# Kernel optimization log

Hardware: AMD Instinct MI355X
Metric: run time of the kernel (lower is better)

## Reference

```python
import jax, jax.numpy as jnp
import numpy as np

HIDDEN = 64
IN_SIZE = 2048 + 512  # sum(obs_shape) + sum(action_shape)


def setup_inputs() -> dict:
    key = jax.random.key(0)
    ks = jax.random.split(key, 10)
    B = 32768
    s_in = 1.0 / np.sqrt(IN_SIZE)
    s_h = 1.0 / np.sqrt(HIDDEN)
    return {
        "state": jax.random.normal(ks[0], (B, 2048), dtype=jnp.float32),
        "action": jax.random.normal(ks[1], (B, 512), dtype=jnp.float32),
        "hidden_state": jax.random.normal(ks[2], (B, HIDDEN), dtype=jnp.float32),
        "cell_state": jax.random.normal(ks[3], (B, HIDDEN), dtype=jnp.float32),
        # fused gate weights, gate order: [i, f, g, o]
        "Wi": jax.random.uniform(ks[4], (IN_SIZE, 4 * HIDDEN), jnp.float32, -s_in, s_in),
        "bi": jax.random.uniform(ks[5], (4 * HIDDEN,), jnp.float32, -s_in, s_in),
        "Wh": jax.random.uniform(ks[6], (HIDDEN, 4 * HIDDEN), jnp.float32, -s_h, s_h),
        "bh": jax.random.uniform(ks[7], (4 * HIDDEN,), jnp.float32, -s_h, s_h),
        "Wo": jax.random.uniform(ks[8], (HIDDEN, 1), jnp.float32, -s_h, s_h),
        "bo": jax.random.uniform(ks[9], (1,), jnp.float32, -s_h, s_h),
    }


def reference(state, action, hidden_state, cell_state, Wi, bi, Wh, bh, Wo, bo):
    x = jnp.concatenate([state, action], axis=1)  # [B, IN_SIZE]
    # two fused GEMMs covering all 8 Linear layers (gate order i,f,g,o)
    gates = x @ Wi + bi + hidden_state @ Wh + bh  # [B, 4*HIDDEN]
    i_t, f_t, g_t, o_t = jnp.split(gates, 4, axis=1)
    i_t = jax.nn.sigmoid(i_t)
    f_t = jax.nn.sigmoid(f_t)
    g_t = jnp.tanh(g_t)
    o_t = jax.nn.sigmoid(o_t)
    c_t = f_t * cell_state + i_t * g_t
    h_t = o_t * jnp.tanh(c_t)
    out = jnp.tanh(h_t @ Wo + bo)  # [B, 1]
    return (out, h_t, c_t)
```

## Files before the change

### kernel.cpp

```cpp
#include <hip/hip_runtime.h>
#include <hip/hip_bf16.h>

#define K_IN 2624
#define NSTEP 82
#define NCHUNK 41

typedef __attribute__((ext_vector_type(8))) short short8;
typedef __attribute__((ext_vector_type(4))) float float4_t;

__device__ __forceinline__ short f2bf(float f) {
    union { __hip_bfloat16 b; short s; } u;
    u.b = __float2bfloat16(f);
    return u.s;
}

__device__ __forceinline__ float sigmoid_fast(float x) {
    return 1.f / (1.f + __expf(-x));
}

__device__ __forceinline__ float tanh_fast(float x) {
    float e = __expf(-2.f * fabsf(x));
    float t = (1.f - e) / (1.f + e);
    return copysignf(t, x);
}

__global__ void prep_kernel(const float* __restrict__ Wi, const float* __restrict__ bi,
                            const float* __restrict__ Wh, const float* __restrict__ bh,
                            short* __restrict__ Wt2, float* __restrict__ bsum) {
    __shared__ short tile[32][264];
    const int t = threadIdx.x;
    const int kb = blockIdx.x;
    const int k0 = kb * 32;

#pragma unroll 8
    for (int j = 0; j < 32; ++j) {
        int k = k0 + j;
        float v = (k < 2560) ? Wi[(size_t)k * 256 + t]
                             : Wh[(size_t)(k - 2560) * 256 + t];
        tile[j][t] = f2bf(v);
    }
    if (kb == 0) bsum[t] = bi[t] + bh[t];
    __syncthreads();

#pragma unroll
    for (int c = 0; c < 4; ++c) {
        int idx = c * 256 + t;
        int lane = idx & 63;
        int nb = idx >> 6;
        int n = nb * 16 + (lane & 15);
        int j0 = (lane >> 4) * 8;
        short8 v;
#pragma unroll
        for (int j = 0; j < 8; ++j) v[j] = tile[j0 + j][n];
        *reinterpret_cast<short8*>(Wt2 + (size_t)kb * 8192 + (size_t)idx * 8) = v;
    }
}

__global__ __launch_bounds__(256, 2)
void lstm_kernel(const float* __restrict__ state, const float* __restrict__ action,
                 const float* __restrict__ hidden, const float* __restrict__ cell,
                 const short* __restrict__ Wt2, const float* __restrict__ bsum,
                 const float* __restrict__ Wo, const float* __restrict__ bo,
                 float* __restrict__ out, int Brows) {
    __shared__ __align__(16) short sB[2 * 16384];

    const int t = threadIdx.x;
    const int w = t >> 6;
    const int l = t & 63;
    const int lr = l & 15;
    const int q = l >> 4;
    const int bm = blockIdx.x;

    const size_t mrow = (size_t)bm * 64 + w * 16 + lr;
    const float* aS = state  + mrow * 2048;
    const float* aA = action + mrow * 512;
    const float* aH = hidden + mrow * 64;

    const short* bg = Wt2 + t * 8;

    float4_t acc[16];
#pragma unroll
    for (int nb = 0; nb < 16; ++nb) acc[nb] = (float4_t)(0.f);

    float4_t aCur[4], aNxt[4], bReg[8];

    auto loadA = [&](int c, float4_t* dst) {
        const float* p; int col;
        if (c < 32)      { p = aS; col = c * 64; }
        else if (c < 40) { p = aA; col = (c - 32) * 64; }
        else             { p = aH; col = 0; }
        dst[0] = *reinterpret_cast<const float4_t*>(p + col + q * 8);
        dst[1] = *reinterpret_cast<const float4_t*>(p + col + q * 8 + 4);
        dst[2] = *reinterpret_cast<const float4_t*>(p + col + 32 + q * 8);
        dst[3] = *reinterpret_cast<const float4_t*>(p + col + 32 + q * 8 + 4);
    };
    auto loadB = [&](int c) {
#pragma unroll
        for (int i = 0; i < 8; ++i)
            bReg[i] = *reinterpret_cast<const float4_t*>(bg + (size_t)c * 16384 + i * 2048);
    };
    auto storeB = [&](int c) {
        short* d = sB + (c & 1) * 16384 + t * 8;
#pragma unroll
        for (int i = 0; i < 8; ++i)
            *reinterpret_cast<float4_t*>(d + i * 2048) = bReg[i];
    };

    loadB(0);
    loadA(0, aCur);
    loadA(1, aNxt);
    storeB(0);
    __syncthreads();

    for (int k = 0; k < NCHUNK; ++k) {
        if (k + 1 < NCHUNK) loadB(k + 1);

        const short* bufr = sB + (k & 1) * 16384;
#pragma unroll
        for (int s = 0; s < 2; ++s) {
            short8 a;
            a[0] = f2bf(aCur[2*s][0]); a[1] = f2bf(aCur[2*s][1]);
            a[2] = f2bf(aCur[2*s][2]); a[3] = f2bf(aCur[2*s][3]);
            a[4] = f2bf(aCur[2*s+1][0]); a[5] = f2bf(aCur[2*s+1][1]);
            a[6] = f2bf(aCur[2*s+1][2]); a[7] = f2bf(aCur[2*s+1][3]);
#pragma unroll
            for (int nb = 0; nb < 16; ++nb) {
                short8 b = *reinterpret_cast<const short8*>(bufr + s * 8192 + nb * 512 + l * 8);
                acc[nb] = __builtin_amdgcn_mfma_f32_16x16x32_bf16(a, b, acc[nb], 0, 0, 0);
            }
        }

#pragma unroll
        for (int i = 0; i < 4; ++i) aCur[i] = aNxt[i];
        if (k + 2 < NCHUNK) loadA(k + 2, aNxt);

        if (k + 1 < NCHUNK) {
            storeB(k + 1);
            __syncthreads();
        }
    }

    __syncthreads();
    float* sG = reinterpret_cast<float*>(sB) + w * 4096;
#pragma unroll
    for (int nb = 0; nb < 16; ++nb)
#pragma unroll
        for (int r = 0; r < 4; ++r)
            sG[(q * 4 + r) * 256 + nb * 16 + lr] = acc[nb][r];
    __syncthreads();

    const float wo = Wo[l];
    const float bov = bo[0];
    const float b0 = bsum[l];
    const float b1 = bsum[64 + l];
    const float b2 = bsum[128 + l];
    const float b3 = bsum[192 + l];
    float* outH = out + Brows;
    float* outC = outH + (size_t)Brows * 64;

#pragma unroll
    for (int r = 0; r < 16; ++r) {
        size_t grow = (size_t)bm * 64 + w * 16 + r;
        float gi = sG[r * 256 + l]       + b0;
        float gf = sG[r * 256 + 64 + l]  + b1;
        float gg = sG[r * 256 + 128 + l] + b2;
        float go = sG[r * 256 + 192 + l] + b3;
        float i_t = sigmoid_fast(gi);
        float f_t = sigmoid_fast(gf);
        float g_t = tanh_fast(gg);
        float o_t = sigmoid_fast(go);
        float c_t = f_t * cell[grow * 64 + l] + i_t * g_t;
        float h_t = o_t * tanh_fast(c_t);
        outC[grow * 64 + l] = c_t;
        outH[grow * 64 + l] = h_t;
        float v = h_t * wo;
#pragma unroll
        for (int off = 32; off > 0; off >>= 1) v += __shfl_down(v, off);
        if (l == 0) out[grow] = tanh_fast(v + bov);
    }
}

extern "C" void kernel_launch(void* const* d_in, const int* in_sizes, int n_in,
                              void* d_out, int out_size, void* d_ws, size_t ws_size,
                              hipStream_t stream) {
    const float* state  = (const float*)d_in[0];
    const float* action = (const float*)d_in[1];
    const float* hidden = (const float*)d_in[2];
    const float* cell   = (const float*)d_in[3];
    const float* Wi     = (const float*)d_in[4];
    const float* bi     = (const float*)d_in[5];
    const float* Wh     = (const float*)d_in[6];
    const float* bh     = (const float*)d_in[7];
    const float* Wo     = (const float*)d_in[8];
    const float* bo     = (const float*)d_in[9];

    const int Brows = in_sizes[0] / 2048;

    short* Wt2  = (short*)d_ws;
    float* bsum = (float*)((char*)d_ws + (size_t)NSTEP * 8192 * sizeof(short));

    prep_kernel<<<NSTEP, 256, 0, stream>>>(Wi, bi, Wh, bh, Wt2, bsum);
    lstm_kernel<<<Brows / 64, 256, 0, stream>>>(state, action, hidden, cell,
                                                Wt2, bsum, Wo, bo, (float*)d_out, Brows);
}
```

Baseline: 462.6 us.

## Stream A and B tiles via async global-to-LDS loads with swizzled layout

Replaces the register-staged loads of activations and weights with direct global_load_lds async copies into double-buffered shared memory, using an XOR swizzle on the fp32 A tile to avoid bank conflicts. The K loop now works on 32-wide chunks with explicit vmcnt waits and barriers. The epilogue applies the gate nonlinearities straight from the MFMA accumulators, with the bias folded into the accumulator init, so the shared-memory gate transpose goes away. The intent is to cut register pressure and VGPR round trips on the memory-bound stream. In exchange the kernel does twice as many barrier-synchronised iterations and relies on hand-placed waitcnt values being correct.

```diff
diff --git a/kernel.cpp b/kernel.cpp
--- a/kernel.cpp
+++ b/kernel.cpp
@@ -3,7 +3,7 @@
 
 #define K_IN 2624
 #define NSTEP 82
-#define NCHUNK 41
+#define NCHUNK 82
 
 typedef __attribute__((ext_vector_type(8))) short short8;
 typedef __attribute__((ext_vector_type(4))) float float4_t;
@@ -22,6 +22,12 @@
     float e = __expf(-2.f * fabsf(x));
     float t = (1.f - e) / (1.f + e);
     return copysignf(t, x);
+}
+
+__device__ __forceinline__ void async16(const void* g, void* l) {
+    __builtin_amdgcn_global_load_lds(
+        (__attribute__((address_space(1))) void*)g,
+        (__attribute__((address_space(3))) void*)l, 16, 0, 0);
 }
 
 __global__ void prep_kernel(const float* __restrict__ Wi, const float* __restrict__ bi,
@@ -62,7 +68,9 @@
                  const short* __restrict__ Wt2, const float* __restrict__ bsum,
                  const float* __restrict__ Wo, const float* __restrict__ bo,
                  float* __restrict__ out, int Brows) {
-    __shared__ __align__(16) short sB[2 * 16384];
+    __shared__ __align__(16) char smem[49152];
+    char* const sA = smem;
+    char* const sB = smem + 16384;
 
     const int t = threadIdx.x;
     const int w = t >> 6;
@@ -71,112 +79,110 @@
     const int q = l >> 4;
     const int bm = blockIdx.x;
 
-    const size_t mrow = (size_t)bm * 64 + w * 16 + lr;
-    const float* aS = state  + mrow * 2048;
-    const float* aA = action + mrow * 512;
-    const float* aH = hidden + mrow * 64;
-
-    const short* bg = Wt2 + t * 8;
+    const int rsub = l >> 3;
+    const int scol = (l & 7) ^ rsub;
+    const char* aSrc[2];
+    auto setA = [&](const float* p, int strideF) {
+#pragma unroll
+        for (int i = 0; i < 2; ++i) {
+            size_t grow = (size_t)bm * 64 + w * 16 + i * 8 + rsub;
+            aSrc[i] = (const char*)(p + grow * (size_t)strideF) + scol * 16;
+        }
+    };
+
+    auto issueAB = [&](int buf, const char* bS) {
+#pragma unroll
+        for (int j = 0; j < 4; ++j)
+            async16(bS + j * 1024, sB + buf * 16384 + (w * 4 + j) * 1024);
+#pragma unroll
+        for (int i = 0; i < 2; ++i) {
+            async16(aSrc[i], sA + buf * 8192 + (w * 16 + i * 8) * 128);
+            aSrc[i] += 128;
+        }
+    };
 
     float4_t acc[16];
 #pragma unroll
-    for (int nb = 0; nb < 16; ++nb) acc[nb] = (float4_t)(0.f);
-
-    float4_t aCur[4], aNxt[4], bReg[8];
-
-    auto loadA = [&](int c, float4_t* dst) {
-        const float* p; int col;
-        if (c < 32)      { p = aS; col = c * 64; }
-        else if (c < 40) { p = aA; col = (c - 32) * 64; }
-        else             { p = aH; col = 0; }
-        dst[0] = *reinterpret_cast<const float4_t*>(p + col + q * 8);
-        dst[1] = *reinterpret_cast<const float4_t*>(p + col + q * 8 + 4);
-        dst[2] = *reinterpret_cast<const float4_t*>(p + col + 32 + q * 8);
-        dst[3] = *reinterpret_cast<const float4_t*>(p + col + 32 + q * 8 + 4);
+    for (int nb = 0; nb < 16; ++nb) acc[nb] = (float4_t)(bsum[nb * 16 + lr]);
+
+    setA(state, 2048);
+    const char* bS0 = (const char*)Wt2 + (w * 4) * 1024 + l * 16;
+    issueAB(0, bS0);
+    issueAB(1, bS0 + 16384);
+    const char* bSn = bS0 + 2 * 16384;
+
+    const char* const sAb = sA + (w * 16 + lr) * 128;
+    const char* const sBb = sB + l * 16;
+    const int g0 = (2 * q) ^ (lr & 7);
+    const int g1 = (2 * q + 1) ^ (lr & 7);
+
+    auto compute = [&](int buf) {
+        const char* bufA = sAb + buf * 8192;
+        const char* bufB = sBb + buf * 16384;
+        float4_t lo = *(const float4_t*)(bufA + g0 * 16);
+        float4_t hi = *(const float4_t*)(bufA + g1 * 16);
+        short8 a;
+        a[0] = f2bf(lo[0]); a[1] = f2bf(lo[1]); a[2] = f2bf(lo[2]); a[3] = f2bf(lo[3]);
+        a[4] = f2bf(hi[0]); a[5] = f2bf(hi[1]); a[6] = f2bf(hi[2]); a[7] = f2bf(hi[3]);
+#pragma unroll
+        for (int nb = 0; nb < 16; ++nb) {
+            short8 b = *(const short8*)(bufB + nb * 1024);
+            acc[nb] = __builtin_amdgcn_mfma_f32_16x16x32_bf16(a, b, acc[nb], 0, 0, 0);
+        }
     };
-    auto loadB = [&](int c) {
-#pragma unroll
-        for (int i = 0; i < 8; ++i)
-            bReg[i] = *reinterpret_cast<const float4_t*>(bg + (size_t)c * 16384 + i * 2048);
-    };
-    auto storeB = [&](int c) {
-        short* d = sB + (c & 1) * 16384 + t * 8;
-#pragma unroll
-        for (int i = 0; i < 8; ++i)
-            *reinterpret_cast<float4_t*>(d + i * 2048) = bReg[i];
-    };
-
-    loadB(0);
-    loadA(0, aCur);
-    loadA(1, aNxt);
-    storeB(0);
-    __syncthreads();
-
-    for (int k = 0; k < NCHUNK; ++k) {
-        if (k + 1 < NCHUNK) loadB(k + 1);
-
-        const short* bufr = sB + (k & 1) * 16384;
-#pragma unroll
-        for (int s = 0; s < 2; ++s) {
-            short8 a;
-            a[0] = f2bf(aCur[2*s][0]); a[1] = f2bf(aCur[2*s][1]);
-            a[2] = f2bf(aCur[2*s][2]); a[3] = f2bf(aCur[2*s][3]);
-            a[4] = f2bf(aCur[2*s+1][0]); a[5] = f2bf(aCur[2*s+1][1]);
-            a[6] = f2bf(aCur[2*s+1][2]); a[7] = f2bf(aCur[2*s+1][3]);
-#pragma unroll
-            for (int nb = 0; nb < 16; ++nb) {
-                short8 b = *reinterpret_cast<const short8*>(bufr + s * 8192 + nb * 512 + l * 8);
-                acc[nb] = __builtin_amdgcn_mfma_f32_16x16x32_bf16(a, b, acc[nb], 0, 0, 0);
-            }
-        }
-
-#pragma unroll
-        for (int i = 0; i < 4; ++i) aCur[i] = aNxt[i];
-        if (k + 2 < NCHUNK) loadA(k + 2, aNxt);
-
-        if (k + 1 < NCHUNK) {
-            storeB(k + 1);
-            __syncthreads();
-        }
-    }
-
-    __syncthreads();
-    float* sG = reinterpret_cast<float*>(sB) + w * 4096;
-#pragma unroll
-    for (int nb = 0; nb < 16; ++nb)
-#pragma unroll
-        for (int r = 0; r < 4; ++r)
-            sG[(q * 4 + r) * 256 + nb * 16 + lr] = acc[nb][r];
-    __syncthreads();
-
-    const float wo = Wo[l];
+
+    for (int k = 0; k < NCHUNK - 1; ++k) {
+        asm volatile("s_waitcnt vmcnt(6)" ::: "memory");
+        __builtin_amdgcn_s_barrier();
+        asm volatile("" ::: "memory");
+        compute(k & 1);
+        asm volatile("" ::: "memory");
+        __builtin_amdgcn_s_barrier();
+        asm volatile("" ::: "memory");
+        const int kk = k + 2;
+        if (kk < NCHUNK) {
+            if (kk == 64) setA(action, 512);
+            if (kk == 80) setA(hidden, 64);
+            issueAB(k & 1, bSn);
+            bSn += 16384;
+        }
+    }
+    asm volatile("s_waitcnt vmcnt(0)" ::: "memory");
+    __builtin_amdgcn_s_barrier();
+    asm volatile("" ::: "memory");
+    compute((NCHUNK - 1) & 1);
+
     const float bov = bo[0];
-    const float b0 = bsum[l];
-    const float b1 = bsum[64 + l];
-    const float b2 = bsum[128 + l];
-    const float b3 = bsum[192 + l];
+    float wo_[4];
+#pragma unroll
+    for (int nb0 = 0; nb0 < 4; ++nb0) wo_[nb0] = Wo[nb0 * 16 + lr];
+
+    const size_t rowbase = (size_t)bm * 64 + w * 16 + q * 4;
     float* outH = out + Brows;
     float* outC = outH + (size_t)Brows * 64;
 
 #pragma unroll
-    for (int r = 0; r < 16; ++r) {
-        size_t grow = (size_t)bm * 64 + w * 16 + r;
-        float gi = sG[r * 256 + l]       + b0;
-        float gf = sG[r * 256 + 64 + l]  + b1;
-        float gg = sG[r * 256 + 128 + l] + b2;
-        float go = sG[r * 256 + 192 + l] + b3;
-        float i_t = sigmoid_fast(gi);
-        float f_t = sigmoid_fast(gf);
-        float g_t = tanh_fast(gg);
-        float o_t = sigmoid_fast(go);
-        float c_t = f_t * cell[grow * 64 + l] + i_t * g_t;
-        float h_t = o_t * tanh_fast(c_t);
-        outC[grow * 64 + l] = c_t;
-        outH[grow * 64 + l] = h_t;
-        float v = h_t * wo;
-#pragma unroll
-        for (int off = 32; off > 0; off >>= 1) v += __shfl_down(v, off);
-        if (l == 0) out[grow] = tanh_fast(v + bov);
+    for (int r = 0; r < 4; ++r) {
+        const size_t grow = rowbase + r;
+        float vpart = 0.f;
+#pragma unroll
+        for (int nb0 = 0; nb0 < 4; ++nb0) {
+            const int n = nb0 * 16 + lr;
+            const float i_t = sigmoid_fast(acc[nb0][r]);
+            const float f_t = sigmoid_fast(acc[nb0 + 4][r]);
+            const float g_t = tanh_fast(acc[nb0 + 8][r]);
+            const float o_t = sigmoid_fast(acc[nb0 + 12][r]);
+            const float c_t = f_t * cell[grow * 64 + n] + i_t * g_t;
+            const float h_t = o_t * tanh_fast(c_t);
+            outC[grow * 64 + n] = c_t;
+            outH[grow * 64 + n] = h_t;
+            vpart += h_t * wo_[nb0];
+        }
+        vpart += __shfl_xor(vpart, 1);
+        vpart += __shfl_xor(vpart, 2);
+        vpart += __shfl_xor(vpart, 4);
+        vpart += __shfl_xor(vpart, 8);
+        if (lr == 0) out[grow] = tanh_fast(vpart + bov);
     }
 }
 
```

Result: faster. 447.9 us (-3.2%).
